# Kernel tuning notes

Hardware: AMD Instinct MI355X
Metric: run time of the kernel (lower is better)

## Reference

```python
import jax, jax.numpy as jnp
import numpy as np

D_MODEL = 2048
NUM_HEADS = 16
D_K = D_MODEL // NUM_HEADS


def _xavier(key, shape):
    # xavier_uniform_ for a (fan_in, fan_out) matrix
    limit = np.sqrt(6.0 / (shape[0] + shape[1]))
    return jax.random.uniform(key, shape, dtype=jnp.float32, minval=-limit, maxval=limit)


def setup_inputs() -> dict:
    key = jax.random.key(0)
    kx, kq, kk, kv, ko = jax.random.split(key, 5)
    x = jax.random.normal(kx, (4, 2048, D_MODEL), dtype=jnp.float32)
    return {
        "x": x,
        "w_q": _xavier(kq, (D_MODEL, D_MODEL)),
        "w_k": _xavier(kk, (D_MODEL, D_MODEL)),
        "w_v": _xavier(kv, (D_MODEL, D_MODEL)),
        "w_o": _xavier(ko, (D_MODEL, D_MODEL)),
    }


def _split_heads(t):
    b, s, _ = t.shape
    return t.reshape(b, s, NUM_HEADS, D_K).transpose(0, 2, 1, 3)  # [b,h,s,dk]


def reference(x, w_q, w_k, w_v, w_o):
    q = _split_heads(x @ w_q)
    k = _split_heads(x @ w_k)
    v = _split_heads(x @ w_v)
    scale = 1.0 / np.sqrt(D_K).astype(np.float32)
    scores = jnp.einsum("bhqd,bhkd->bhqk", q, k) * scale
    attn = jax.nn.softmax(scores, axis=-1)
    out = jnp.einsum("bhqk,bhkd->bhqd", attn, v)  # [b,h,s,dk]
    b, h, s, dk = out.shape
    out = out.transpose(0, 2, 1, 3).reshape(b, s, h * dk)
    return out @ w_o
```

## Files before the change

### kernel.cpp

```cpp
#include <hip/hip_runtime.h>
#include <hip/hip_bf16.h>

typedef __attribute__((ext_vector_type(8))) __bf16 bf16x8;
typedef __attribute__((ext_vector_type(4))) float f32x4;
typedef __attribute__((ext_vector_type(16))) float f32x16;
typedef __attribute__((ext_vector_type(8))) unsigned short u16x8;
typedef unsigned short u16;

#define DEVINL static __device__ __forceinline__

namespace {
constexpr int kB = 4;
constexpr int kS = 2048;
constexpr int kDM = 2048;
constexpr int kH = 16;
constexpr int kDK = 128;
constexpr int kM = kB * kS;
constexpr int kNQKV = 3 * kDM;
constexpr float kE2 = 0.08838834764831845f * 1.44269504088896f;
}

DEVINL u16 f2bf(float f) {
  __hip_bfloat16 h = __float2bfloat16(f);
  return __builtin_bit_cast(u16, h);
}

#if __has_builtin(__builtin_amdgcn_exp2f)
DEVINL float exp2_fast(float x) { return __builtin_amdgcn_exp2f(x); }
#else
DEVINL float exp2_fast(float x) { return exp2f(x); }
#endif

#define GLOAD16(gp, lp) \
  __builtin_amdgcn_global_load_lds((const __attribute__((address_space(1))) void*)(gp), \
                                   (__attribute__((address_space(3))) void*)(lp), 16, 0, 0)

DEVINL bf16x8 lds_frag(const u16* p) { return *reinterpret_cast<const bf16x8*>(p); }

DEVINL f32x4 MFMA16x16(bf16x8 a, bf16x8 b, f32x4 c) {
  return __builtin_amdgcn_mfma_f32_16x16x32_bf16(a, b, c, 0, 0, 0);
}

struct TrueT { static constexpr bool value = true; };
struct FalseT { static constexpr bool value = false; };

__global__ __launch_bounds__(256) void cast_x_kernel(const float* __restrict__ x,
                                                     u16* __restrict__ o, int n4) {
  int i = blockIdx.x * 256 + threadIdx.x;
  if (i >= n4) return;
  float4 v = reinterpret_cast<const float4*>(x)[i];
  ushort4 r;
  r.x = f2bf(v.x); r.y = f2bf(v.y); r.z = f2bf(v.z); r.w = f2bf(v.w);
  reinterpret_cast<ushort4*>(o)[i] = r;
}

__global__ __launch_bounds__(256) void transpose_w_kernel(const float* __restrict__ w0,
    const float* __restrict__ w1, const float* __restrict__ w2, const float* __restrict__ w3,
    u16* __restrict__ wtcat, u16* __restrict__ wot) {
  const float* src = (blockIdx.z == 0) ? w0 : (blockIdx.z == 1) ? w1
                    : (blockIdx.z == 2) ? w2 : w3;
  u16* dst = (blockIdx.z < 3) ? (wtcat + (size_t)blockIdx.z * kDM * kDM) : wot;
  __shared__ float tile[32][33];
  int n0 = blockIdx.x * 32, k0 = blockIdx.y * 32;
  int tx = threadIdx.x, ty = threadIdx.y;
#pragma unroll
  for (int i = 0; i < 4; ++i)
    tile[ty + i * 8][tx] = src[(size_t)(k0 + ty + i * 8) * kDM + n0 + tx];
  __syncthreads();
#pragma unroll
  for (int i = 0; i < 4; ++i)
    dst[(size_t)(n0 + ty + i * 8) * kDM + k0 + tx] = f2bf(tile[tx][ty + i * 8]);
}

DEVINL void cstore(float* p, float v) { *p = v; }
DEVINL void cstore(u16* p, float v) { *p = f2bf(v); }

#define PH_OPEN()                                      \
  __builtin_amdgcn_sched_barrier(0);                   \
  __builtin_amdgcn_s_barrier();                        \
  asm volatile("s_waitcnt lgkmcnt(0)" ::: "memory");   \
  __builtin_amdgcn_sched_barrier(0);                   \
  __builtin_amdgcn_s_setprio(1)

#define PH_CLOSE()                                     \
  __builtin_amdgcn_s_setprio(0);                       \
  __builtin_amdgcn_sched_barrier(0);                   \
  __builtin_amdgcn_s_barrier()

#define PH_CLOSE_G4()                                  \
  __builtin_amdgcn_s_setprio(0);                       \
  __builtin_amdgcn_sched_barrier(0);                   \
  asm volatile("s_waitcnt vmcnt(4)" ::: "memory");     \
  __builtin_amdgcn_sched_barrier(0);                   \
  __builtin_amdgcn_s_barrier()

#define PH_CLOSE_G0()                                  \
  __builtin_amdgcn_s_setprio(0);                       \
  __builtin_amdgcn_sched_barrier(0);                   \
  asm volatile("s_waitcnt vmcnt(0)" ::: "memory");     \
  __builtin_amdgcn_sched_barrier(0);                   \
  __builtin_amdgcn_s_barrier()

#define RD_A(SB, MQ, DST)                                             \
  do {                                                                \
    _Pragma("unroll") for (int mf = 0; mf < 4; ++mf) {                \
      const u16* p_ = (SB) + (awrow + (MQ) * 64 + mf * 16) * 64;      \
      DST[mf * 2 + 0] = lds_frag(p_ + g0);                            \
      DST[mf * 2 + 1] = lds_frag(p_ + g1);                            \
    }                                                                 \
  } while (0)

#define RD_BH(SB, NH)                                                 \
  do {                                                                \
    _Pragma("unroll") for (int nf = 0; nf < 2; ++nf) {                \
      const u16* p_ = (SB) + (bwrow + (NH) * 32 + nf * 16) * 64;      \
      b[(NH) * 4 + nf * 2 + 0] = lds_frag(p_ + g0);                   \
      b[(NH) * 4 + nf * 2 + 1] = lds_frag(p_ + g1);                   \
    }                                                                 \
  } while (0)

#define MMQ(MQ, NH, AF)                                               \
  do {                                                                \
    _Pragma("unroll") for (int mf = 0; mf < 4; ++mf)                  \
      _Pragma("unroll") for (int nf = 0; nf < 2; ++nf) {              \
        f32x4 t_ = acc[(MQ) * 4 + mf][(NH) * 2 + nf];                 \
        t_ = MFMA16x16(AF[mf * 2 + 0], b[(NH) * 4 + nf * 2 + 0], t_); \
        t_ = MFMA16x16(AF[mf * 2 + 1], b[(NH) * 4 + nf * 2 + 1], t_); \
        acc[(MQ) * 4 + mf][(NH) * 2 + nf] = t_;                       \
      }                                                               \
  } while (0)

#define STG_A(buf, R0, kt) \
  GLOAD16(baseA + (size_t)(R0) * lda + (size_t)(kt) * 64, ldsA + (buf) * 16384 + (R0) * 64)
#define STG_B(buf, R0, kt) \
  GLOAD16(baseB + (size_t)(R0) * ldb + (size_t)(kt) * 64, ldsB + (buf) * 16384 + (R0) * 64)

template <typename CT, bool WRITEV>
__global__ __launch_bounds__(512, 2) void gemm256_kernel(const u16* __restrict__ A,
    const u16* __restrict__ Bt, CT* __restrict__ C, u16* __restrict__ Vt,
    int K, int lda, int ldb, int ldc) {
  __shared__ __align__(16) u16 sA[2][16384];
  __shared__ __align__(16) u16 sB[2][16384];
  const int tid = threadIdx.x;
  const int lane = tid & 63, wid = tid >> 6;
  const int r15 = lane & 15, hi = lane >> 4;
  const int wm = wid >> 2, wn = wid & 3;

  const int gx = gridDim.x, nwg = gx * gridDim.y;
  const int orig = blockIdx.y * gx + blockIdx.x;
  const int wg = (orig & 7) * (nwg >> 3) + (orig >> 3);
  const int n0 = (wg % gx) * 256;
  const int m0 = (wg / gx) * 256;

  const int NT = K >> 6;
  const int NITER = NT >> 1;

  const int rc = tid >> 3;
  const int cg = (tid & 7) ^ (rc & 7);
  const u16* baseA = A + (size_t)(m0 + rc) * lda + cg * 8;
  const u16* baseB = Bt + (size_t)(n0 + rc) * ldb + cg * 8;
  u16* ldsA = &sA[0][0] + rc * 64 + (tid & 7) * 8;
  u16* ldsB = &sB[0][0] + rc * 64 + (tid & 7) * 8;

  const int sw = r15 & 7;
  const int g0 = (hi ^ sw) * 8;
  const int g1 = ((4 + hi) ^ sw) * 8;
  const int awrow = wm * 128 + r15;
  const int bwrow = wn * 64 + r15;
  const u16* sA0 = &sA[0][0]; const u16* sA1 = &sA[1][0];
  const u16* sB0 = &sB[0][0]; const u16* sB1 = &sB[1][0];

  f32x4 acc[8][4] = {};
  bf16x8 aE[8], aO[8], b[8];

  STG_A(0, 0, 0); STG_A(0, 64, 0); STG_A(0, 128, 0); STG_A(0, 192, 0);
  STG_B(0, 0, 0); STG_B(0, 64, 0); STG_B(0, 128, 0); STG_B(0, 192, 0);
  STG_A(1, 0, 1); STG_A(1, 128, 1);
  STG_B(1, 0, 1); STG_B(1, 64, 1); STG_B(1, 128, 1); STG_B(1, 192, 1);
  asm volatile("s_waitcnt vmcnt(6)" ::: "memory");
  __builtin_amdgcn_sched_barrier(0);
  __builtin_amdgcn_s_barrier();
  RD_A(sA0, 0, aE); RD_BH(sB0, 0);

  int kb = 0;
  auto iter = [&](auto lastc) {
    constexpr bool L = decltype(lastc)::value;
    const int kO = kb + 1, k2 = kb + 2, k3 = kb + 3;
    STG_A(1, 64, kO); STG_A(1, 192, kO);
    PH_OPEN();
    RD_BH(sB0, 1);
    MMQ(0, 0, aE);
    PH_CLOSE();
    if constexpr (!L) { STG_A(0, 0, k2); STG_A(0, 128, k2); }
    PH_OPEN();
    RD_A(sA0, 1, aO);
    MMQ(0, 1, aE);
    PH_CLOSE();
    if constexpr (!L) { STG_B(0, 0, k2); STG_B(0, 64, k2); }
    PH_OPEN();
    MMQ(1, 0, aO);
    if constexpr (L) { PH_CLOSE_G0(); } else { PH_CLOSE_G4(); }
    if constexpr (!L) { STG_B(0, 128, k2); STG_B(0, 192, k2); }
    PH_OPEN();
    RD_A(sA1, 0, aE); RD_BH(sB1, 0);
    MMQ(1, 1, aO);
    PH_CLOSE();
    if constexpr (!L) { STG_A(0, 64, k2); STG_A(0, 192, k2); }
    PH_OPEN();
    RD_BH(sB1, 1);
    MMQ(0, 0, aE);
    PH_CLOSE();
    if constexpr (!L) { STG_A(1, 0, k3); STG_A(1, 128, k3); }
    PH_OPEN();
    RD_A(sA1, 1, aO);
    MMQ(0, 1, aE);
    PH_CLOSE();
    if constexpr (!L) { STG_B(1, 0, k3); STG_B(1, 64, k3); }
    PH_OPEN();
    MMQ(1, 0, aO);
    if constexpr (L) { PH_CLOSE_G0(); } else { PH_CLOSE_G4(); }
    if constexpr (!L) { STG_B(1, 128, k3); STG_B(1, 192, k3); }
    PH_OPEN();
    if constexpr (!L) { RD_A(sA0, 0, aE); RD_BH(sB0, 0); }
    MMQ(1, 1, aO);
    PH_CLOSE();
    kb += 2;
  };
  for (int i = 0; i < NITER - 1; ++i) iter(FalseT{});
  iter(TrueT{});

  if constexpr (WRITEV) {
    if (n0 >= 2 * kDM) {
      const int hswap = ((hi & 1) << 1) | (hi >> 1);
#pragma unroll
      for (int im = 0; im < 8; ++im) {
        const int m_base = m0 + wm * 128 + im * 16;
        const int bq = m_base >> 11;
        const int sp = (m_base & (kS - 1)) + hswap * 4;
#pragma unroll
        for (int in = 0; in < 4; ++in) {
          const int c = n0 - 2 * kDM + wn * 64 + in * 16 + r15;
          const int hh = c >> 7, dd = c & 127;
          u16* dst = Vt + ((size_t)((bq * kH + hh) * kDK + dd)) * kS + sp;
          ushort4 pk;
          pk.x = f2bf(acc[im][in][0]); pk.y = f2bf(acc[im][in][1]);
          pk.z = f2bf(acc[im][in][2]); pk.w = f2bf(acc[im][in][3]);
          *reinterpret_cast<ushort4*>(dst) = pk;
        }
      }
      return;
    }
  }
  const size_t crow0 = (size_t)(m0 + wm * 128 + hi * 4);
  const int col0 = n0 + wn * 64 + r15;
#pragma unroll
  for (int im = 0; im < 8; ++im)
#pragma unroll
    for (int in = 0; in < 4; ++in)
#pragma unroll
      for (int r = 0; r < 4; ++r)
        cstore(&C[(crow0 + im * 16 + r) * ldc + col0 + in * 16], acc[im][in][r]);
}

__global__ __launch_bounds__(256, 2) void attn_kernel(const u16* __restrict__ qkv,
    const u16* __restrict__ vt, u16* __restrict__ attn_out) {
  __shared__ __align__(16) u16 lds[2][16384];
  const int tid = threadIdx.x;
  const int lane = tid & 63, wid = tid >> 6;
  const int l31 = lane & 31, hi5 = lane >> 5;
  const int q0 = blockIdx.x * 128, h = blockIdx.y, b = blockIdx.z;
  const int bh = b * kH + h;

  const int krow = tid >> 4, kg = tid & 15;
  const u16* kp = qkv + (size_t)(b * kS + krow) * kNQKV + kDM + h * kDK
                  + (size_t)((kg ^ (krow & 7)) * 8);
  const int vrow = tid >> 3, vg = tid & 7;
  const u16* vp = vt + (size_t)(bh * kDK + vrow) * kS + (size_t)((vg ^ (vrow & 7)) * 8);

  auto stage_kv = [&](u16* dst) {
#pragma unroll
    for (int i = 0; i < 4; ++i)
      GLOAD16(kp + (size_t)i * 16 * kNQKV, dst + (tid + 256 * i) * 8);
#pragma unroll
    for (int i = 0; i < 4; ++i)
      GLOAD16(vp + (size_t)i * 32 * kS, dst + 8192 + (tid + 256 * i) * 8);
    kp += (size_t)64 * kNQKV;
    vp += 64;
  };

#pragma unroll
  for (int i = 0; i < 8; ++i) {
    int row = (tid >> 4) + 16 * i;
    GLOAD16(qkv + (size_t)(b * kS + q0 + row) * kNQKV + h * kDK
                + (size_t)(((tid & 15) ^ (row & 7)) * 8),
            (u16*)lds[1] + (tid + 256 * i) * 8);
  }
  stage_kv(lds[0]);
  __syncthreads();

  bf16x8 qf[8];
  {
    const int qrow = wid * 32 + l31;
    const u16* qb = (const u16*)lds[1];
#pragma unroll
    for (int ds = 0; ds < 8; ++ds) {
      int slot = (ds * 2 + hi5) ^ (qrow & 7);
      qf[ds] = lds_frag(&qb[qrow * 128 + slot * 8]);
    }
  }
  __syncthreads();

  f32x16 o[4] = {};
  float mi = -1e30f, li = 0.f;
  int cur = 0;

  for (int t = 0; t < kS / 64; ++t) {
    if (t < kS / 64 - 1) stage_kv(lds[cur ^ 1]);

    const u16* Kb = (const u16*)lds[cur];
    const u16* Vb = Kb + 8192;

    f32x16 s0 = {}, s1 = {};
    const int kr = l31;
#pragma unroll
    for (int ds = 0; ds < 8; ++ds) {
      int slot = ((ds * 2 + hi5) ^ (kr & 7)) * 8;
      bf16x8 k0 = lds_frag(&Kb[kr * 128 + slot]);
      bf16x8 k1 = lds_frag(&Kb[(32 + kr) * 128 + slot]);
      s0 = __builtin_amdgcn_mfma_f32_32x32x16_bf16(k0, qf[ds], s0, 0, 0, 0);
      s1 = __builtin_amdgcn_mfma_f32_32x32x16_bf16(k1, qf[ds], s1, 0, 0, 0);
    }

    float mx = s0[0];
#pragma unroll
    for (int r = 1; r < 16; ++r) mx = fmaxf(mx, s0[r]);
#pragma unroll
    for (int r = 0; r < 16; ++r) mx = fmaxf(mx, s1[r]);
    mx = fmaxf(mx, __shfl_xor(mx, 32));
    float mc = mx * kE2;
    if (__any(mc > mi + 8.0f)) {
      float mn = fmaxf(mi, mc);
      float corr = exp2_fast(mi - mn);
      mi = mn;
      li *= corr;
#pragma unroll
      for (int r = 0; r < 16; ++r) {
        float c = __shfl(corr, (r & 3) + 8 * (r >> 2) + 4 * hi5);
        o[0][r] *= c; o[1][r] *= c; o[2][r] *= c; o[3][r] *= c;
      }
    }
    float p0[16], p1[16];
    float rs = 0.f;
#pragma unroll
    for (int r = 0; r < 16; ++r) { p0[r] = exp2_fast(s0[r] * kE2 - mi); rs += p0[r]; }
#pragma unroll
    for (int r = 0; r < 16; ++r) { p1[r] = exp2_fast(s1[r] * kE2 - mi); rs += p1[r]; }
    rs += __shfl_xor(rs, 32);
    li += rs;

    u16x8 pw0, pw1, pw2, pw3;
#pragma unroll
    for (int r = 0; r < 8; ++r) {
      pw0[r] = f2bf(p0[r]);
      pw1[r] = f2bf(p0[r + 8]);
      pw2[r] = f2bf(p1[r]);
      pw3[r] = f2bf(p1[r + 8]);
    }
    bf16x8 pa[4] = {__builtin_bit_cast(bf16x8, pw0), __builtin_bit_cast(bf16x8, pw1),
                    __builtin_bit_cast(bf16x8, pw2), __builtin_bit_cast(bf16x8, pw3)};

#pragma unroll
    for (int dt = 0; dt < 4; ++dt) {
      const int row = dt * 32 + l31;
      const int rs8 = row & 7;
#pragma unroll
      for (int ks = 0; ks < 4; ++ks) {
        bf16x8 bv = lds_frag(&Vb[row * 64 + ((ks * 2 + hi5) ^ rs8) * 8]);
        o[dt] = __builtin_amdgcn_mfma_f32_32x32x16_bf16(pa[ks], bv, o[dt], 0, 0, 0);
      }
    }

    __syncthreads();
    cur ^= 1;
  }

  float rli = 1.0f / li;
  const size_t obase = (size_t)(b * kS + q0 + wid * 32) * kDM + h * kDK + l31;
#pragma unroll
  for (int r = 0; r < 16; ++r) {
    int ql = (r & 3) + 8 * (r >> 2) + 4 * hi5;
    float w = __shfl(rli, ql);
#pragma unroll
    for (int dt = 0; dt < 4; ++dt)
      attn_out[obase + (size_t)ql * kDM + dt * 32] = f2bf(o[dt][r] * w);
  }
}

extern "C" void kernel_launch(void* const* d_in, const int* in_sizes, int n_in,
                              void* d_out, int out_size, void* d_ws, size_t ws_size,
                              hipStream_t stream) {
  (void)in_sizes; (void)n_in; (void)out_size; (void)ws_size;
  const float* x  = (const float*)d_in[0];
  const float* wq = (const float*)d_in[1];
  const float* wk = (const float*)d_in[2];
  const float* wv = (const float*)d_in[3];
  const float* wo = (const float*)d_in[4];

  char* p = (char*)d_ws;
  u16* xb   = (u16*)p; p += (size_t)kM * kDM * 2;
  u16* wtc  = (u16*)p; p += (size_t)kNQKV * kDM * 2;
  u16* wot  = (u16*)p; p += (size_t)kDM * kDM * 2;
  u16* qkvb = (u16*)p; p += (size_t)kM * kNQKV * 2;
  u16* vtb  = (u16*)p; p += (size_t)kB * kH * kDK * kS * 2;
  u16* aob  = xb;

  int n4 = kM * kDM / 4;
  cast_x_kernel<<<(n4 + 255) / 256, 256, 0, stream>>>(x, xb, n4);
  transpose_w_kernel<<<dim3(kDM / 32, kDM / 32, 4), dim3(32, 8), 0, stream>>>(
      wq, wk, wv, wo, wtc, wot);
  gemm256_kernel<u16, true><<<dim3(kNQKV / 256, kM / 256), 512, 0, stream>>>(
      xb, wtc, qkvb, vtb, kDM, kDM, kDM, kNQKV);
  attn_kernel<<<dim3(kS / 128, kH, kB), 256, 0, stream>>>(qkvb, vtb, aob);
  gemm256_kernel<float, false><<<dim3(kDM / 256, kM / 256), 512, 0, stream>>>(
      aob, wot, (float*)d_out, nullptr, kDM, kDM, kDM, kDM);
}
```

Before: 440.4 us.

## Halve per-phase barriers in the GEMM main loop and delay LDS staging one phase

Drops the closing s_barrier from each compute phase, so every phase has a single barrier at entry. To keep the LDS double buffers safe with fewer barriers, each global-to-LDS staging load moves one phase later. The vmcnt gates now sit right after the relevant staging loads. The aim is less barrier stall time between MFMA phases. The risk is a write-after-read race on shared memory if any staging load now overlaps with reads still in flight in other waves.

```diff
diff --git a/kernel.cpp b/kernel.cpp
--- a/kernel.cpp
+++ b/kernel.cpp
@@ -75,31 +75,24 @@
 DEVINL void cstore(float* p, float v) { *p = v; }
 DEVINL void cstore(u16* p, float v) { *p = f2bf(v); }
 
-#define PH_OPEN()                                      \
+#define PH_BEGIN()                                     \
   __builtin_amdgcn_sched_barrier(0);                   \
   __builtin_amdgcn_s_barrier();                        \
   asm volatile("s_waitcnt lgkmcnt(0)" ::: "memory");   \
   __builtin_amdgcn_sched_barrier(0);                   \
   __builtin_amdgcn_s_setprio(1)
 
-#define PH_CLOSE()                                     \
+#define PH_END()                                       \
   __builtin_amdgcn_s_setprio(0);                       \
-  __builtin_amdgcn_sched_barrier(0);                   \
-  __builtin_amdgcn_s_barrier()
-
-#define PH_CLOSE_G4()                                  \
-  __builtin_amdgcn_s_setprio(0);                       \
-  __builtin_amdgcn_sched_barrier(0);                   \
+  __builtin_amdgcn_sched_barrier(0)
+
+#define GATE4() \
   asm volatile("s_waitcnt vmcnt(4)" ::: "memory");     \
-  __builtin_amdgcn_sched_barrier(0);                   \
-  __builtin_amdgcn_s_barrier()
-
-#define PH_CLOSE_G0()                                  \
-  __builtin_amdgcn_s_setprio(0);                       \
-  __builtin_amdgcn_sched_barrier(0);                   \
+  __builtin_amdgcn_sched_barrier(0)
+
+#define GATE0() \
   asm volatile("s_waitcnt vmcnt(0)" ::: "memory");     \
-  __builtin_amdgcn_sched_barrier(0);                   \
-  __builtin_amdgcn_s_barrier()
+  __builtin_amdgcn_sched_barrier(0)
 
 #define RD_A(SB, MQ, DST)                                             \
   do {                                                                \
@@ -186,44 +179,46 @@
   auto iter = [&](auto lastc) {
     constexpr bool L = decltype(lastc)::value;
     const int kO = kb + 1, k2 = kb + 2, k3 = kb + 3;
-    STG_A(1, 64, kO); STG_A(1, 192, kO);
-    PH_OPEN();
+    PH_BEGIN();
     RD_BH(sB0, 1);
     MMQ(0, 0, aE);
-    PH_CLOSE();
-    if constexpr (!L) { STG_A(0, 0, k2); STG_A(0, 128, k2); }
-    PH_OPEN();
+    PH_END();
+    STG_A(1, 64, kO); STG_A(1, 192, kO);
+    PH_BEGIN();
     RD_A(sA0, 1, aO);
     MMQ(0, 1, aE);
-    PH_CLOSE();
-    if constexpr (!L) { STG_B(0, 0, k2); STG_B(0, 64, k2); }
-    PH_OPEN();
+    PH_END();
+    if constexpr (!L) { STG_A(0, 0, k2); STG_A(0, 128, k2); }
+    PH_BEGIN();
     MMQ(1, 0, aO);
-    if constexpr (L) { PH_CLOSE_G0(); } else { PH_CLOSE_G4(); }
-    if constexpr (!L) { STG_B(0, 128, k2); STG_B(0, 192, k2); }
-    PH_OPEN();
+    PH_END();
+    if constexpr (!L) { STG_B(0, 0, k2); STG_B(0, 64, k2); GATE4(); }
+    else              { GATE0(); }
+    PH_BEGIN();
     RD_A(sA1, 0, aE); RD_BH(sB1, 0);
     MMQ(1, 1, aO);
-    PH_CLOSE();
-    if constexpr (!L) { STG_A(0, 64, k2); STG_A(0, 192, k2); }
-    PH_OPEN();
+    PH_END();
+    if constexpr (!L) { STG_B(0, 128, k2); STG_B(0, 192, k2); }
+    PH_BEGIN();
     RD_BH(sB1, 1);
     MMQ(0, 0, aE);
-    PH_CLOSE();
-    if constexpr (!L) { STG_A(1, 0, k3); STG_A(1, 128, k3); }
-    PH_OPEN();
+    PH_END();
+    if constexpr (!L) { STG_A(0, 64, k2); STG_A(0, 192, k2); }
+    PH_BEGIN();
     RD_A(sA1, 1, aO);
     MMQ(0, 1, aE);
-    PH_CLOSE();
-    if constexpr (!L) { STG_B(1, 0, k3); STG_B(1, 64, k3); }
-    PH_OPEN();
+    PH_END();
+    if constexpr (!L) { STG_A(1, 0, k3); STG_A(1, 128, k3); }
+    PH_BEGIN();
     MMQ(1, 0, aO);
-    if constexpr (L) { PH_CLOSE_G0(); } else { PH_CLOSE_G4(); }
-    if constexpr (!L) { STG_B(1, 128, k3); STG_B(1, 192, k3); }
-    PH_OPEN();
+    PH_END();
+    if constexpr (!L) { STG_B(1, 0, k3); STG_B(1, 64, k3); GATE4(); }
+    else              { GATE0(); }
+    PH_BEGIN();
     if constexpr (!L) { RD_A(sA0, 0, aE); RD_BH(sB0, 0); }
     MMQ(1, 1, aO);
-    PH_CLOSE();
+    PH_END();
+    if constexpr (!L) { STG_B(1, 128, k3); STG_B(1, 192, k3); }
     kb += 2;
   };
   for (int i = 0; i < NITER - 1; ++i) iter(FalseT{});
```

New measurement: 436.3 us. About the same (-0.9%).
